# Kernel optimization log

Measured on AMD Instinct MI355X. Metric: run time of the kernel, lower is better.

The kernel has to match this reference:

```python
import jax, jax.numpy as jnp
import numpy as np

HEADS = 8
DIM_HEAD = 64


def setup_inputs() -> dict:
    key = jax.random.key(0)
    ks = jax.random.split(key, 5)
    B, N, C, coor = 2, 2048, 256, 3
    dim_inner = HEADS * DIM_HEAD  # 512
    # weight scale 1/16 ~ 1/sqrt(256) keeps softmax logits in a sane range
    w_scale = 1.0 / 16.0
    return {
        "x": jax.random.normal(ks[0], (B, N, C, coor), dtype=jnp.float32),
        "Wq": jax.random.normal(ks[1], (dim_inner, C), dtype=jnp.float32) * w_scale,
        "Wk": jax.random.normal(ks[2], (dim_inner, C), dtype=jnp.float32) * w_scale,
        "Wv": jax.random.normal(ks[3], (dim_inner, C), dtype=jnp.float32) * w_scale,
        "Wo": jax.random.normal(ks[4], (C, dim_inner), dtype=jnp.float32) * w_scale,
    }


def _split_heads(t, B, N, coor):
    # b n (h d) c -> b h n (d c)
    t = t.reshape(B, N, HEADS, DIM_HEAD, coor)
    t = t.transpose(0, 2, 1, 3, 4)
    return t.reshape(B, HEADS, N, DIM_HEAD * coor)


def reference(x, Wq, Wk, Wv, Wo):
    B, N, C, coor = x.shape
    # VNLinear: einsum('... i c, o i -> ... o c')
    q = jnp.einsum('bnic,oi->bnoc', x, Wq)
    k = jnp.einsum('bnic,oi->bnoc', x, Wk)
    v = jnp.einsum('bnic,oi->bnoc', x, Wv)
    q = _split_heads(q, B, N, coor)  # (B, H, N, d*c)
    k = _split_heads(k, B, N, coor)
    v = _split_heads(v, B, N, coor)
    scale = (DIM_HEAD * coor) ** -0.5
    sim = jnp.einsum('bhie,bhje->bhij', q, k) * scale  # (B, H, N, N)
    attn = jax.nn.softmax(sim, axis=-1)
    out = jnp.einsum('bhij,bhje->bhie', attn, v)  # (B, H, N, d*c)
    # b h n (d c) -> b n (h d) c
    out = out.reshape(B, HEADS, N, DIM_HEAD, coor).transpose(0, 2, 1, 3, 4)
    out = out.reshape(B, N, HEADS * DIM_HEAD, coor)
    # to_out VNLinear
    return jnp.einsum('bnic,oi->bnoc', out, Wo)  # (B, N, C, 3)
```

## Files before the change

### kernel.cpp

```cpp
#include <hip/hip_runtime.h>

#define HEADS 8
#define DH 64
#define CO 3
#define E 192
#define NSEQ 2048
#define BATCH 2
#define CIN 256
#define DINNER 512
#define NTOK 4096
#define BHTOT 16

typedef __attribute__((ext_vector_type(8))) short bf16x8;
typedef __attribute__((ext_vector_type(4))) short bf16x4;
typedef __attribute__((ext_vector_type(4))) float f32x4;

static __device__ inline short f2bf(float f) {
  union { float f; unsigned u; } v; v.f = f;
  unsigned r = (v.u + 0x7FFFu + ((v.u >> 16) & 1u)) >> 16;
  return (short)r;
}

static __device__ inline void load_lds16(const short* g, short* l) {
  __builtin_amdgcn_global_load_lds(
      (const __attribute__((address_space(1))) void*)g,
      (__attribute__((address_space(3))) void*)l, 16, 0, 0);
}


__global__ __launch_bounds__(256) void prep(const float* __restrict__ x,
                                            const float* __restrict__ Wq,
                                            const float* __restrict__ Wk,
                                            const float* __restrict__ Wv,
                                            const float* __restrict__ Wo,
                                            short* __restrict__ xcp,
                                            short* __restrict__ wqkvp,
                                            short* __restrict__ wop) {
  int gid = blockIdx.x * 256 + threadIdx.x;
  if (gid < NTOK * CIN) {
    int t = gid >> 8, i = gid & 255;
    const float* p = x + (size_t)gid * 3;
    float a = p[0], b = p[1], c = p[2];
    int mt = t >> 4, ln = t & 15, ks = i >> 5, qd = (i >> 3) & 3, j = i & 7;
    size_t inner = (size_t)(qd * 16 + ln) * 8 + j;
    xcp[((size_t)(0 * 256 + mt) * 8 + ks) * 512 + inner] = f2bf(a);
    xcp[((size_t)(1 * 256 + mt) * 8 + ks) * 512 + inner] = f2bf(b);
    xcp[((size_t)(2 * 256 + mt) * 8 + ks) * 512 + inner] = f2bf(c);
    return;
  }
  int idx = gid - NTOK * CIN;
  const float qscale = 0.07216878364870323f * 1.4426950408889634f;
  if (idx < 1536 * 256) {
    int o = idx >> 8, i = idx & 255;
    float v;
    if (o < 512) v = Wq[idx] * qscale;
    else if (o < 1024) v = Wk[idx - 512 * 256];
    else v = Wv[idx - 1024 * 256];
    int nt = o >> 4, ln = o & 15, ks = i >> 5, qd = (i >> 3) & 3, j = i & 7;
    wqkvp[((size_t)(nt * 8 + ks)) * 512 + (qd * 16 + ln) * 8 + j] = f2bf(v);
  } else {
    int j0 = idx - 1536 * 256;
    if (j0 < 256 * 512) {
      int o2 = j0 >> 9, i = j0 & 511;
      int nt = o2 >> 4, ln = o2 & 15, ks = i >> 5, qd = (i >> 3) & 3, j = i & 7;
      wop[((size_t)(nt * 16 + ks)) * 512 + (qd * 16 + ln) * 8 + j] = f2bf(Wo[j0]);
    }
  }
}

__global__ __launch_bounds__(256, 4) void qkv_gemm(const short* __restrict__ xcp,
                                                   const short* __restrict__ wqkvp,
                                                   short* __restrict__ qp,
                                                   short* __restrict__ kp,
                                                   short* __restrict__ vp) {
  __shared__ __align__(16) short pool[17408];
  int c = blockIdx.z, ntb = blockIdx.x, mtb = blockIdx.y;
  int tid = threadIdx.x, wave = tid >> 6, lane = tid & 63;
  int ln = lane & 15, quad = lane >> 4;
  int wm = wave >> 1, wn = wave & 1;

  const short* gA = xcp + ((size_t)(c * 256 + mtb * 8) * 8) * 512;
  const short* gB = wqkvp + ((size_t)(ntb * 8) * 8) * 512;

  f32x4 acc[4][4] = {};
#pragma unroll
  for (int i = 0; i < 2; i++) {
    int q = tid + 256 * i, mf = q >> 6, l = q & 63;
    load_lds16(gA + (size_t)(mf * 8) * 512 + l * 8, pool + q * 8);
  }
  for (int ks = 0; ks < 8; ks++) {
    int b = ks & 1;
    __syncthreads();
    if (ks < 7) {
#pragma unroll
      for (int i = 0; i < 2; i++) {
        int q = tid + 256 * i, mf = q >> 6, l = q & 63;
        load_lds16(gA + (size_t)(mf * 8 + ks + 1) * 512 + l * 8,
                   pool + (b ^ 1) * 4096 + q * 8);
      }
    }
    const short* As = pool + b * 4096;
    bf16x8 af[4], bfr[4];
#pragma unroll
    for (int j = 0; j < 4; j++)
      bfr[j] = *(const bf16x8*)(gB + (size_t)((wn * 4 + j) * 8 + ks) * 512 + lane * 8);
#pragma unroll
    for (int i = 0; i < 4; i++) af[i] = *(const bf16x8*)&As[(wm * 4 + i) * 512 + lane * 8];
#pragma unroll
    for (int i = 0; i < 4; i++)
#pragma unroll
      for (int j = 0; j < 4; j++)
        acc[i][j] = __builtin_amdgcn_mfma_f32_16x16x32_bf16(af[i], bfr[j], acc[i][j], 0, 0, 0);
  }

  int mat = ntb >> 2;
  int b0 = mtb >> 4;
  if (mat < 2) {
    __syncthreads();
    short* tp = pool;
#pragma unroll
    for (int i = 0; i < 4; i++)
#pragma unroll
      for (int j = 0; j < 4; j++)
#pragma unroll
        for (int jj = 0; jj < 4; jj++)
          tp[(wm * 64 + i * 16 + quad * 4 + jj) * 136 + wn * 64 + j * 16 + ln] =
              f2bf(acc[i][j][jj]);
    __syncthreads();
    short* dst = (mat == 0) ? qp : kp;
    int h0 = (ntb & 3) * 2;
#pragma unroll
    for (int rep = 0; rep < 8; rep++) {
      int gi = rep * 256 + tid;
      int l2 = gi & 15, qd = (gi >> 4) & 3, nf2 = (gi >> 6) & 3,
          esp = (gi >> 8) & 1, hh = (gi >> 9) & 1, kt2 = gi >> 10;
      int tl = kt2 * 64 + nf2 * 16 + l2;
      bf16x8 val = *(const bf16x8*)&tp[tl * 136 + hh * 64 + (esp * 4 + qd) * 8];
      int bhx = b0 * 8 + h0 + hh;
      int kt = (mtb * 2 + kt2) & 31;
      int es = c * 2 + esp;
      size_t off = (((size_t)((bhx * 32 + kt) * 24) + es * 4 + nf2) * 64 +
                    (size_t)(qd * 16 + l2)) * 8;
      *(bf16x8*)(dst + off) = val;
    }
  } else {
#pragma unroll
    for (int i = 0; i < 4; i++) {
      int kt = (mtb * 2 + wm) & 31;
      int ks2 = (i >> 1) & 1;
      int qd2 = (i * 2 + (quad >> 1)) & 3;
#pragma unroll
      for (int j = 0; j < 4; j++) {
        int o = ntb * 128 + wn * 64 + j * 16 + ln;
        int oo = o & 511, h = oo >> 6, d = oo & 63;
        int ef = c * 4 + (d >> 4), l2v = d & 15;
        int bhx = b0 * 8 + h;
        size_t off = ((size_t)((bhx * 32 + kt) * 24 + ks2 * 12 + ef)) * 512 +
                     (qd2 * 16 + l2v) * 8 + (quad & 1) * 4;
        bf16x4 val = { f2bf(acc[i][j][0]), f2bf(acc[i][j][1]),
                       f2bf(acc[i][j][2]), f2bf(acc[i][j][3]) };
        *(bf16x4*)(vp + off) = val;
      }
    }
  }
}

__global__ __launch_bounds__(256, 2) void attn(const short* __restrict__ qp,
                                               const short* __restrict__ kp,
                                               const short* __restrict__ vp,
                                               short* __restrict__ opart,
                                               float* __restrict__ lpart) {
  __shared__ __align__(16) short pool[33792];
  int pair = blockIdx.x, qt = blockIdx.y;
  int bh = pair & 15, kh = pair >> 4;
  int tid = threadIdx.x, wave = tid >> 6, lane = tid & 63;
  int ln = lane & 15, quad = lane >> 4;
  short* Kl = pool;
  short* Vl = pool + 12288;
  short* Pl = pool + 24576;

  bf16x8 qf[2][6];
#pragma unroll
  for (int rg = 0; rg < 2; rg++) {
    int fi = wave * 2 + rg;
    const short* qb = qp +
        ((size_t)(bh * 32 + qt * 2 + (fi >> 2)) * 24 + (fi & 3)) * 512 + lane * 8;
#pragma unroll
    for (int es = 0; es < 6; es++) qf[rg][es] = *(const bf16x8*)(qb + es * 2048);
  }

  float l_r[2][4] = {};
  f32x4 acc[2][12] = {};
  const short* gKb = kp + (size_t)(bh * 32 + kh * 16) * 12288;
  const short* gVb = vp + (size_t)(bh * 32 + kh * 16) * 12288;

  for (int kt = 0; kt < 16; kt++) {
    const short* gK = gKb + (size_t)kt * 12288;
    const short* gV = gVb + (size_t)kt * 12288;
#pragma unroll
    for (int i = 0; i < 6; i++) {
      load_lds16(gK + (i * 256 + tid) * 8, Kl + (i * 256 + tid) * 8);
      load_lds16(gV + (i * 256 + tid) * 8, Vl + (i * 256 + tid) * 8);
    }
    __syncthreads();

    f32x4 s[2][4];
#pragma unroll
    for (int nf = 0; nf < 4; nf++) {
      f32x4 a0 = {}, a1 = {};
#pragma unroll
      for (int es = 0; es < 6; es++) {
        bf16x8 kf = *(const bf16x8*)&Kl[(es * 4 + nf) * 512 + lane * 8];
        a0 = __builtin_amdgcn_mfma_f32_16x16x32_bf16(qf[0][es], kf, a0, 0, 0, 0);
        a1 = __builtin_amdgcn_mfma_f32_16x16x32_bf16(qf[1][es], kf, a1, 0, 0, 0);
      }
      s[0][nf] = a0; s[1][nf] = a1;
    }

#pragma unroll
    for (int rg = 0; rg < 2; rg++)
#pragma unroll
      for (int jj = 0; jj < 4; jj++)
#pragma unroll
        for (int nf = 0; nf < 4; nf++) {
          float p = __builtin_amdgcn_exp2f(s[rg][nf][jj]);
          union { float f; unsigned u; } v; v.f = p;
          Pl[((wave * 2 + rg) * 16 + quad * 4 + jj) * 72 + nf * 16 + ln] =
              (short)((v.u + 0x8000u) >> 16);
          l_r[rg][jj] += p;
        }

    bf16x8 pa[2][2];
#pragma unroll
    for (int rg = 0; rg < 2; rg++) {
      const short* pb = &Pl[((wave * 2 + rg) * 16 + ln) * 72 + quad * 8];
      pa[rg][0] = *(const bf16x8*)pb;
      pa[rg][1] = *(const bf16x8*)(pb + 32);
    }
#pragma unroll
    for (int ef = 0; ef < 12; ef++) {
      bf16x8 v0 = *(const bf16x8*)&Vl[ef * 512 + lane * 8];
      bf16x8 v1 = *(const bf16x8*)&Vl[(12 + ef) * 512 + lane * 8];
#pragma unroll
      for (int rg = 0; rg < 2; rg++) {
        acc[rg][ef] = __builtin_amdgcn_mfma_f32_16x16x32_bf16(pa[rg][0], v0, acc[rg][ef], 0, 0, 0);
        acc[rg][ef] = __builtin_amdgcn_mfma_f32_16x16x32_bf16(pa[rg][1], v1, acc[rg][ef], 0, 0, 0);
      }
    }
    __syncthreads();
  }

#pragma unroll
  for (int rg = 0; rg < 2; rg++)
#pragma unroll
    for (int jj = 0; jj < 4; jj++)
#pragma unroll
      for (int off = 1; off < 16; off <<= 1)
        l_r[rg][jj] += __shfl_xor(l_r[rg][jj], off, 64);

  short* tp = pool;
#pragma unroll
  for (int rg = 0; rg < 2; rg++)
#pragma unroll
    for (int jj = 0; jj < 4; jj++) {
      int row = (wave * 2 + rg) * 16 + quad * 4 + jj;
#pragma unroll
      for (int ef = 0; ef < 12; ef++)
        tp[row * 200 + ef * 16 + ln] = f2bf(acc[rg][ef][jj]);
    }
  __syncthreads();
  const size_t obase = ((size_t)(kh * 16 + bh) * 2048 + qt * 128) * 192;
#pragma unroll
  for (int rep = 0; rep < 12; rep++) {
    int gi = rep * 256 + tid;
    int row = gi / 24, c8 = gi - row * 24;
    *(bf16x8*)(opart + obase + (size_t)row * 192 + c8 * 8) =
        *(const bf16x8*)&tp[row * 200 + c8 * 8];
  }
  int lb = (kh * 16 + bh) * 2048 + qt * 128;
  if (ln == 0) {
#pragma unroll
    for (int rg = 0; rg < 2; rg++)
#pragma unroll
      for (int jj = 0; jj < 4; jj++)
        lpart[lb + (wave * 2 + rg) * 16 + quad * 4 + jj] = l_r[rg][jj];
  }
}

__global__ __launch_bounds__(256) void merge(const short* __restrict__ opart,
                                             const float* __restrict__ lpart,
                                             short* __restrict__ owp) {
  int G = blockIdx.x * 256 + threadIdx.x;
  int inner = G & 63, qd = inner >> 4, row16 = inner & 15;
  int ks = (G >> 6) & 15, h = ks >> 1, esp = ks & 1;
  int mt = (G >> 10) & 255;
  int c = G >> 18;
  int t = mt * 16 + row16, b = t >> 11, n = t & 2047;
  int bh = b * 8 + h;
  size_t so = ((size_t)bh * 2048 + n) * 192 + c * 64 + esp * 32 + qd * 8;
  const size_t HSTR = (size_t)16 * 2048 * 192;
  bf16x8 o1 = *(const bf16x8*)(opart + so);
  bf16x8 o2 = *(const bf16x8*)(opart + HSTR + so);
  float l = lpart[bh * 2048 + n] + lpart[32768 + bh * 2048 + n];
  float inv = 1.f / l;
  bf16x8 r;
#pragma unroll
  for (int j = 0; j < 8; j++) {
    union { unsigned u; float f; } a, b2;
    a.u = ((unsigned)(unsigned short)o1[j]) << 16;
    b2.u = ((unsigned)(unsigned short)o2[j]) << 16;
    r[j] = f2bf((a.f + b2.f) * inv);
  }
  *(bf16x8*)(owp + (size_t)G * 8) = r;
}

__global__ __launch_bounds__(256, 4) void out_gemm(const short* __restrict__ owp,
                                                   const short* __restrict__ wop,
                                                   float* __restrict__ out) {
  __shared__ __align__(16) short Al[2048], Bl[2048];
  int c = blockIdx.z, ntb = blockIdx.x, mtb = blockIdx.y;
  int tid = threadIdx.x, wave = tid >> 6, lane = tid & 63;
  int ln = lane & 15, quad = lane >> 4;
  int wm = wave >> 1, wn = wave & 1;

  f32x4 acc[2][2] = {};
  const short* gAb = owp + ((size_t)(c * 256 + mtb * 4) * 16) * 512;
  const short* gBb = wop + ((size_t)(ntb * 4) * 16) * 512;
  for (int ks = 0; ks < 16; ks++) {
    {
      int mf = tid >> 6, l = tid & 63;
      load_lds16(gAb + (size_t)(mf * 16 + ks) * 512 + l * 8, &Al[tid * 8]);
      load_lds16(gBb + (size_t)(mf * 16 + ks) * 512 + l * 8, &Bl[tid * 8]);
    }
    __syncthreads();
    bf16x8 af[2], bfr[2];
#pragma unroll
    for (int i = 0; i < 2; i++) af[i] = *(const bf16x8*)&Al[(wm * 2 + i) * 512 + lane * 8];
#pragma unroll
    for (int j = 0; j < 2; j++) bfr[j] = *(const bf16x8*)&Bl[(wn * 2 + j) * 512 + lane * 8];
#pragma unroll
    for (int i = 0; i < 2; i++)
#pragma unroll
      for (int j = 0; j < 2; j++)
        acc[i][j] = __builtin_amdgcn_mfma_f32_16x16x32_bf16(af[i], bfr[j], acc[i][j], 0, 0, 0);
    __syncthreads();
  }
#pragma unroll
  for (int i = 0; i < 2; i++) {
#pragma unroll
    for (int j = 0; j < 2; j++) {
      int o2 = ntb * 64 + (wn * 2 + j) * 16 + ln;
#pragma unroll
      for (int jj = 0; jj < 4; jj++) {
        int t = mtb * 64 + (wm * 2 + i) * 16 + quad * 4 + jj;
        out[((size_t)t * 256 + o2) * 3 + c] = acc[i][j][jj];
      }
    }
  }
}

extern "C" void kernel_launch(void* const* d_in, const int* in_sizes, int n_in,
                              void* d_out, int out_size, void* d_ws, size_t ws_size,
                              hipStream_t stream) {
  const float* x  = (const float*)d_in[0];
  const float* Wq = (const float*)d_in[1];
  const float* Wk = (const float*)d_in[2];
  const float* Wv = (const float*)d_in[3];
  const float* Wo = (const float*)d_in[4];
  float* out = (float*)d_out;

  short* ws    = (short*)d_ws;
  short* xcp   = ws;
  short* wqkvp = xcp + 3 * NTOK * CIN;
  short* wop   = wqkvp + 1536 * 256;
  short* qp    = wop + 256 * 512;
  short* kp    = qp + (size_t)BHTOT * NSEQ * E;
  short* vp    = kp + (size_t)BHTOT * NSEQ * E;
  short* opart = vp + (size_t)BHTOT * NSEQ * E;
  float* lpart = (float*)xcp;
  short* owp   = qp;

  prep<<<6144, 256, 0, stream>>>(x, Wq, Wk, Wv, Wo, xcp, wqkvp, wop);
  qkv_gemm<<<dim3(12, 32, 3), 256, 0, stream>>>(xcp, wqkvp, qp, kp, vp);
  attn<<<dim3(32, 16), 256, 0, stream>>>(qp, kp, vp, opart, lpart);
  merge<<<3072, 256, 0, stream>>>(opart, lpart, owp);
  out_gemm<<<dim3(4, 64, 3), 256, 0, stream>>>(owp, wop, out);
}
```

Baseline: 166.5 us.

## Fuse split-KV merge into output GEMM and coalesce x repack via LDS

The separate merge kernel that combined the two KV-split partial outputs and normalized by the softmax sum is folded into the output projection GEMM. Each block now builds its 16-row A tile in LDS directly from opart/lpart and computes all 256 output channels, reading Wo fragments straight from global memory. The prep kernel also stages each 16-token x tile through shared memory with float4 loads and writes bf16x8 vectors, replacing scattered scalar stores. This removes one launch and an intermediate write/read, but gives the GEMM smaller M tiles with uncached B loads from global.

After: 162.7 us. 2.3% less time.

```diff
diff --git a/kernel.cpp b/kernel.cpp
--- a/kernel.cpp
+++ b/kernel.cpp
@@ -14,11 +14,18 @@
 typedef __attribute__((ext_vector_type(8))) short bf16x8;
 typedef __attribute__((ext_vector_type(4))) short bf16x4;
 typedef __attribute__((ext_vector_type(4))) float f32x4;
+typedef __attribute__((ext_vector_type(4))) float float4v;
 
 static __device__ inline short f2bf(float f) {
   union { float f; unsigned u; } v; v.f = f;
   unsigned r = (v.u + 0x7FFFu + ((v.u >> 16) & 1u)) >> 16;
   return (short)r;
+}
+
+static __device__ inline float bf2f(short s) {
+  union { unsigned u; float f; } a;
+  a.u = ((unsigned)(unsigned short)s) << 16;
+  return a.f;
 }
 
 static __device__ inline void load_lds16(const short* g, short* l) {
@@ -36,19 +43,36 @@
                                             short* __restrict__ xcp,
                                             short* __restrict__ wqkvp,
                                             short* __restrict__ wop) {
-  int gid = blockIdx.x * 256 + threadIdx.x;
-  if (gid < NTOK * CIN) {
-    int t = gid >> 8, i = gid & 255;
-    const float* p = x + (size_t)gid * 3;
-    float a = p[0], b = p[1], c = p[2];
-    int mt = t >> 4, ln = t & 15, ks = i >> 5, qd = (i >> 3) & 3, j = i & 7;
-    size_t inner = (size_t)(qd * 16 + ln) * 8 + j;
-    xcp[((size_t)(0 * 256 + mt) * 8 + ks) * 512 + inner] = f2bf(a);
-    xcp[((size_t)(1 * 256 + mt) * 8 + ks) * 512 + inner] = f2bf(b);
-    xcp[((size_t)(2 * 256 + mt) * 8 + ks) * 512 + inner] = f2bf(c);
+  int tid = threadIdx.x;
+  if (blockIdx.x < 256) {
+    __shared__ short st[12288];
+    int mt = blockIdx.x;
+    const float* xb = x + (size_t)mt * 12288;
+#pragma unroll
+    for (int r = 0; r < 12; r++) {
+      int idx4 = r * 256 + tid;
+      float4v v = *(const float4v*)(xb + idx4 * 4);
+#pragma unroll
+      for (int e = 0; e < 4; e++) {
+        int fp = idx4 * 4 + e;
+        int ti = fp / 3, c = fp - ti * 3;
+        int tl = ti >> 8, i = ti & 255;
+        int ks = i >> 5, qd = (i >> 3) & 3, j = i & 7;
+        st[c * 4096 + ks * 512 + (qd * 16 + tl) * 8 + j] = f2bf(v[e]);
+      }
+    }
+    __syncthreads();
+    short* dst = xcp;
+#pragma unroll
+    for (int rep = 0; rep < 6; rep++) {
+      int g = rep * 256 + tid;
+      int c = g >> 9, rem = g & 511;
+      *(bf16x8*)(dst + ((size_t)(c * 256 + mt) * 8) * 512 + rem * 8) =
+          *(const bf16x8*)&st[c * 4096 + rem * 8];
+    }
     return;
   }
-  int idx = gid - NTOK * CIN;
+  int idx = (blockIdx.x - 256) * 256 + tid;
   const float qscale = 0.07216878364870323f * 1.4426950408889634f;
   if (idx < 1536 * 256) {
     int o = idx >> 8, i = idx & 255;
@@ -287,74 +311,53 @@
   }
 }
 
-__global__ __launch_bounds__(256) void merge(const short* __restrict__ opart,
-                                             const float* __restrict__ lpart,
-                                             short* __restrict__ owp) {
-  int G = blockIdx.x * 256 + threadIdx.x;
-  int inner = G & 63, qd = inner >> 4, row16 = inner & 15;
-  int ks = (G >> 6) & 15, h = ks >> 1, esp = ks & 1;
-  int mt = (G >> 10) & 255;
-  int c = G >> 18;
-  int t = mt * 16 + row16, b = t >> 11, n = t & 2047;
-  int bh = b * 8 + h;
-  size_t so = ((size_t)bh * 2048 + n) * 192 + c * 64 + esp * 32 + qd * 8;
-  const size_t HSTR = (size_t)16 * 2048 * 192;
-  bf16x8 o1 = *(const bf16x8*)(opart + so);
-  bf16x8 o2 = *(const bf16x8*)(opart + HSTR + so);
-  float l = lpart[bh * 2048 + n] + lpart[32768 + bh * 2048 + n];
-  float inv = 1.f / l;
-  bf16x8 r;
-#pragma unroll
-  for (int j = 0; j < 8; j++) {
-    union { unsigned u; float f; } a, b2;
-    a.u = ((unsigned)(unsigned short)o1[j]) << 16;
-    b2.u = ((unsigned)(unsigned short)o2[j]) << 16;
-    r[j] = f2bf((a.f + b2.f) * inv);
-  }
-  *(bf16x8*)(owp + (size_t)G * 8) = r;
-}
-
-__global__ __launch_bounds__(256, 4) void out_gemm(const short* __restrict__ owp,
+__global__ __launch_bounds__(256, 4) void out_gemm(const short* __restrict__ opart,
+                                                   const float* __restrict__ lpart,
                                                    const short* __restrict__ wop,
                                                    float* __restrict__ out) {
-  __shared__ __align__(16) short Al[2048], Bl[2048];
-  int c = blockIdx.z, ntb = blockIdx.x, mtb = blockIdx.y;
+  __shared__ __align__(16) short Al[8192];
+  int mtb = blockIdx.x, c = blockIdx.y;
   int tid = threadIdx.x, wave = tid >> 6, lane = tid & 63;
   int ln = lane & 15, quad = lane >> 4;
-  int wm = wave >> 1, wn = wave & 1;
-
-  f32x4 acc[2][2] = {};
-  const short* gAb = owp + ((size_t)(c * 256 + mtb * 4) * 16) * 512;
-  const short* gBb = wop + ((size_t)(ntb * 4) * 16) * 512;
+  const size_t HSTR = (size_t)16 * 2048 * 192;
+
+#pragma unroll
+  for (int rep = 0; rep < 4; rep++) {
+    int g = rep * 256 + tid;
+    int d8 = g & 7, h = (g >> 3) & 7, row16 = g >> 6;
+    int t = mtb * 16 + row16, b = t >> 11, n = t & 2047;
+    int bh = b * 8 + h;
+    size_t src = ((size_t)bh * 2048 + n) * 192 + c * 64 + d8 * 8;
+    bf16x8 o1 = *(const bf16x8*)(opart + src);
+    bf16x8 o2 = *(const bf16x8*)(opart + HSTR + src);
+    float l = lpart[bh * 2048 + n] + lpart[32768 + bh * 2048 + n];
+    float inv = 1.f / l;
+    bf16x8 r;
+#pragma unroll
+    for (int j = 0; j < 8; j++) r[j] = f2bf((bf2f(o1[j]) + bf2f(o2[j])) * inv);
+    int i0 = h * 64 + d8 * 8;
+    int ks = i0 >> 5, qd = d8 & 3;
+    *(bf16x8*)&Al[ks * 512 + (qd * 16 + row16) * 8] = r;
+  }
+  __syncthreads();
+
+  f32x4 acc[4] = {};
   for (int ks = 0; ks < 16; ks++) {
-    {
-      int mf = tid >> 6, l = tid & 63;
-      load_lds16(gAb + (size_t)(mf * 16 + ks) * 512 + l * 8, &Al[tid * 8]);
-      load_lds16(gBb + (size_t)(mf * 16 + ks) * 512 + l * 8, &Bl[tid * 8]);
-    }
-    __syncthreads();
-    bf16x8 af[2], bfr[2];
-#pragma unroll
-    for (int i = 0; i < 2; i++) af[i] = *(const bf16x8*)&Al[(wm * 2 + i) * 512 + lane * 8];
-#pragma unroll
-    for (int j = 0; j < 2; j++) bfr[j] = *(const bf16x8*)&Bl[(wn * 2 + j) * 512 + lane * 8];
-#pragma unroll
-    for (int i = 0; i < 2; i++)
-#pragma unroll
-      for (int j = 0; j < 2; j++)
-        acc[i][j] = __builtin_amdgcn_mfma_f32_16x16x32_bf16(af[i], bfr[j], acc[i][j], 0, 0, 0);
-    __syncthreads();
-  }
-#pragma unroll
-  for (int i = 0; i < 2; i++) {
-#pragma unroll
-    for (int j = 0; j < 2; j++) {
-      int o2 = ntb * 64 + (wn * 2 + j) * 16 + ln;
-#pragma unroll
-      for (int jj = 0; jj < 4; jj++) {
-        int t = mtb * 64 + (wm * 2 + i) * 16 + quad * 4 + jj;
-        out[((size_t)t * 256 + o2) * 3 + c] = acc[i][j][jj];
-      }
+    bf16x8 af = *(const bf16x8*)&Al[ks * 512 + lane * 8];
+#pragma unroll
+    for (int jf = 0; jf < 4; jf++) {
+      int nt = wave * 4 + jf;
+      bf16x8 bfr = *(const bf16x8*)(wop + (size_t)(nt * 16 + ks) * 512 + lane * 8);
+      acc[jf] = __builtin_amdgcn_mfma_f32_16x16x32_bf16(af, bfr, acc[jf], 0, 0, 0);
+    }
+  }
+#pragma unroll
+  for (int jf = 0; jf < 4; jf++) {
+    int o2 = (wave * 4 + jf) * 16 + ln;
+#pragma unroll
+    for (int jj = 0; jj < 4; jj++) {
+      int t = mtb * 16 + quad * 4 + jj;
+      out[((size_t)t * 256 + o2) * 3 + c] = acc[jf][jj];
     }
   }
 }
@@ -378,11 +381,9 @@
   short* vp    = kp + (size_t)BHTOT * NSEQ * E;
   short* opart = vp + (size_t)BHTOT * NSEQ * E;
   float* lpart = (float*)xcp;
-  short* owp   = qp;
-
-  prep<<<6144, 256, 0, stream>>>(x, Wq, Wk, Wv, Wo, xcp, wqkvp, wop);
+
+  prep<<<2304, 256, 0, stream>>>(x, Wq, Wk, Wv, Wo, xcp, wqkvp, wop);
   qkv_gemm<<<dim3(12, 32, 3), 256, 0, stream>>>(xcp, wqkvp, qp, kp, vp);
   attn<<<dim3(32, 16), 256, 0, stream>>>(qp, kp, vp, opart, lpart);
-  merge<<<3072, 256, 0, stream>>>(opart, lpart, owp);
-  out_gemm<<<dim3(4, 64, 3), 256, 0, stream>>>(owp, wop, out);
-}
+  out_gemm<<<dim3(256, 3), 256, 0, stream>>>(opart, lpart, wop, out);
+}
```
